# Performance work log

Measured on AMD Instinct MI355X. Metric: run time of the kernel, lower is better.

## Reference

```python
import jax, jax.numpy as jnp
import numpy as np

B, L, DM, DI, N = 8, 2048, 512, 768, 8  # batch, seq, d_model, d_inner=int(1.5*512), d_state


def setup_inputs() -> dict:
    key = jax.random.key(0)
    ks = jax.random.split(key, 8)
    g = lambda k, shape, sc=1.0: (jax.random.normal(k, shape, jnp.float32) * sc)
    return {
        "x": g(ks[0], (B, L, DM)),
        "W_in": g(ks[1], (DM, 2 * DI), 0.02),    # in_proj weight (stored in->out)
        "A_log": g(ks[2], (DI, N)),               # nn.Parameter(randn)
        "D_param": g(ks[3], (DI,)),               # skip-connection D
        "W_x": g(ks[4], (DI, N), 0.02),           # x_proj weight
        "W_dt": g(ks[5], (N, DI), 0.02),          # dt_proj weight
        "b_dt": jnp.zeros((DI,), jnp.float32),    # dt_proj bias
        "W_out": g(ks[6], (DI, DM), 0.02),        # out_proj weight
    }


def reference(x, W_in, A_log, D_param, W_x, W_dt, b_dt, W_out):
    xz = x @ W_in                                  # (B,L,2*DI)
    d_inner = W_in.shape[1] // 2
    x_ssm, z = xz[..., :d_inner], xz[..., d_inner:]
    x_ssm = jax.nn.silu(x_ssm)                     # (B,L,DI)
    A = -jnp.exp(A_log.astype(jnp.float32))        # (DI,N)
    delta = jax.nn.softplus((x_ssm @ W_x) @ W_dt + b_dt)  # (B,L,DI)

    n_state = A.shape[-1]

    def step(h, inp):
        xt, dt = inp                               # each (B,DI)
        dA = jnp.exp(dt[..., None] * A)            # (B,DI,N)
        h = dA * h + dt[..., None] * xt[..., None]
        y = jnp.sum(h, axis=-1) + D_param * xt     # (B,DI)
        return h, y

    h0 = jnp.zeros((x.shape[0], d_inner, n_state), x_ssm.dtype)
    xs = (jnp.swapaxes(x_ssm, 0, 1), jnp.swapaxes(delta, 0, 1))  # (L,B,DI)
    _, ys = jax.lax.scan(step, h0, xs)             # ys: (L,B,DI)
    y = jnp.swapaxes(ys, 0, 1)                     # (B,L,DI)
    y = y * jax.nn.silu(z)
    return y @ W_out                               # (B,L,DM)
```

## Files before the change

### kernel.cpp

```cpp
#include <hip/hip_runtime.h>

typedef unsigned short bfu;
typedef __attribute__((ext_vector_type(8))) short short8;
typedef __attribute__((ext_vector_type(4))) float f32x4;

__device__ __forceinline__ float bf2f(bfu u){
  union { unsigned int i; float f; } v; v.i = ((unsigned int)u) << 16; return v.f;
}
__device__ __forceinline__ bfu f2bf(float f){
  union { float f; unsigned int i; } v; v.f = f;
  unsigned int r = (v.i + 0x7FFFu + ((v.i >> 16) & 1u)) >> 16;
  return (bfu)r;
}
__device__ __forceinline__ float fexp2(float x){ return __builtin_amdgcn_exp2f(x); }
__device__ __forceinline__ float flog2(float x){ return __builtin_amdgcn_logf(x); }
__device__ __forceinline__ float softplusf(float x){
  float t = fexp2(-fabsf(x) * 1.44269504088896f);
  return fmaxf(x, 0.f) + 0.69314718055995f * flog2(1.f + t);
}
__device__ __forceinline__ void gload16(const bfu* g, bfu* l){
  __builtin_amdgcn_global_load_lds((const __attribute__((address_space(1))) unsigned int*)g,
                                   (__attribute__((address_space(3))) unsigned int*)l, 16, 0, 0);
}

__global__ __launch_bounds__(256) void cvt_all_kernel(const float* __restrict__ x, bfu* __restrict__ x_bf,
                                                      const float* __restrict__ W_in, const float* __restrict__ W_out,
                                                      const float* __restrict__ W_x,
                                                      bfu* __restrict__ WinT, bfu* __restrict__ WoutT,
                                                      float* __restrict__ WxT){
  int g = blockIdx.x * 256 + threadIdx.x;
  if (g < 2097152){
    float4 v = ((const float4*)x)[g];
    ushort4 o;
    o.x = f2bf(v.x); o.y = f2bf(v.y); o.z = f2bf(v.z); o.w = f2bf(v.w);
    ((ushort4*)x_bf)[g] = o;
    return;
  }
  int h = g - 2097152;
  if (h < 786432){
    int r = h % 512, c = h / 512;
    WinT[h] = f2bf(W_in[(size_t)r * 1536 + c]);
  } else if (h < 786432 + 393216){
    int h2 = h - 786432;
    int r = h2 % 768, c = h2 / 768;
    WoutT[h2] = f2bf(W_out[(size_t)r * 512 + c]);
  } else if (h < 786432 + 393216 + 6144){
    int h2 = h - (786432 + 393216);
    int n = h2 / 768, k = h2 % 768;
    WxT[h2] = W_x[(size_t)k * 8 + n];
  }
}

template<int EPI, int BM, int KK>
__global__ __launch_bounds__(BM * 2)
void gemm_sb(const bfu* __restrict__ Amat, const bfu* __restrict__ Bt,
             void* __restrict__ out0, void* __restrict__ out1,
             int NBN, int N)
{
  constexpr int BN = 128;
  constexpr int THREADS = BM * 2;
  constexpr int RPI = THREADS / 8;
  __shared__ bfu As[BM * 64];
  __shared__ bfu Bs[BN * 64];
  const int tid  = threadIdx.x;
  const int lane = tid & 63;
  const int w    = tid >> 6;
  const int wr   = w >> 1, wc = w & 1;

  const int cpx = gridDim.x >> 3;
  const int id  = blockIdx.x;
  const int nid = (id & 7) * cpx + (id >> 3);
  const int bn  = nid % NBN;
  const int bm  = nid / NBN;

  const int srow = tid >> 3;
  const int scol = ((tid & 7) ^ (srow & 7)) * 8;
  const bfu* gA = Amat + ((size_t)(bm * BM + srow)) * KK + scol;
  const bfu* gB = Bt   + ((size_t)(bn * BN + srow)) * KK + scol;
  bfu* lA = As + srow * 64 + (tid & 7) * 8;
  bfu* lB = Bs + srow * 64 + (tid & 7) * 8;

  f32x4 acc[4][4];
  #pragma unroll
  for (int i = 0; i < 4; i++)
    #pragma unroll
    for (int j = 0; j < 4; j++)
      #pragma unroll
      for (int r = 0; r < 4; r++) acc[i][j][r] = 0.f;

  for (int k0 = 0; k0 < KK; k0 += 64){
    #pragma unroll
    for (int i = 0; i < BM / RPI; i++)
      gload16(gA + (size_t)(i * RPI) * KK + k0, lA + i * RPI * 64);
    #pragma unroll
    for (int j = 0; j < BN / RPI; j++)
      gload16(gB + (size_t)(j * RPI) * KK + k0, lB + j * RPI * 64);
    __syncthreads();

    #pragma unroll
    for (int kk = 0; kk < 2; kk++){
      short8 a[4], b[4];
      const int sA = ((kk * 4 + (lane >> 4)) ^ (lane & 7)) * 8;
      #pragma unroll
      for (int m = 0; m < 4; m++){
        int r = wr * 64 + m * 16 + (lane & 15);
        a[m] = *(const short8*)&As[r * 64 + sA];
      }
      #pragma unroll
      for (int n = 0; n < 4; n++){
        int r = wc * 64 + n * 16 + (lane & 15);
        b[n] = *(const short8*)&Bs[r * 64 + sA];
      }
      #pragma unroll
      for (int m = 0; m < 4; m++)
        #pragma unroll
        for (int n = 0; n < 4; n++)
          acc[m][n] = __builtin_amdgcn_mfma_f32_16x16x32_bf16(a[m], b[n], acc[m][n], 0, 0, 0);
    }
    __syncthreads();
  }

  #pragma unroll
  for (int m = 0; m < 4; m++){
    #pragma unroll
    for (int n = 0; n < 4; n++){
      const int row0 = bm * BM + wr * 64 + m * 16 + (lane >> 4) * 4;
      const int col  = bn * BN + wc * 64 + n * 16 + (lane & 15);
      #pragma unroll
      for (int r = 0; r < 4; r++){
        float v = acc[m][n][r];
        int row = row0 + r;
        if (EPI == 0){
          float s = v / (1.f + __expf(-v));
          if (col < 768) ((bfu*)out0)[(size_t)row * 768 + col]         = f2bf(s);
          else           ((bfu*)out1)[(size_t)row * 768 + (col - 768)] = f2bf(s);
        } else {
          ((float*)out0)[(size_t)row * N + col] = v;
        }
      }
    }
  }
}

__global__ __launch_bounds__(256) void u_kernel(const bfu* __restrict__ xssm, const float* __restrict__ WxT,
                                                float* __restrict__ u){
  int wid = threadIdx.x >> 6, lane = threadIdx.x & 63;
  int row = blockIdx.x * 4 + wid;
  const bfu* xr = xssm + (size_t)row * 768;
  float acc[8];
  #pragma unroll
  for (int n = 0; n < 8; n++) acc[n] = 0.f;
  #pragma unroll
  for (int i = 0; i < 3; i++){
    int kb = i * 256 + lane * 4;
    ushort4 xq = *(const ushort4*)(xr + kb);
    float x0 = bf2f(xq.x), x1 = bf2f(xq.y), x2 = bf2f(xq.z), x3 = bf2f(xq.w);
    #pragma unroll
    for (int n = 0; n < 8; n++){
      float4 wv = *(const float4*)(WxT + (size_t)n * 768 + kb);
      acc[n] += x0 * wv.x + x1 * wv.y + x2 * wv.z + x3 * wv.w;
    }
  }
  #pragma unroll
  for (int n = 0; n < 8; n++){
    #pragma unroll
    for (int off = 32; off >= 1; off >>= 1) acc[n] += __shfl_xor(acc[n], off, 64);
  }
  if (lane == 0){
    float4 o0 = { acc[0], acc[1], acc[2], acc[3] };
    float4 o1 = { acc[4], acc[5], acc[6], acc[7] };
    *(float4*)(u + (size_t)row * 8)     = o0;
    *(float4*)(u + (size_t)row * 8 + 4) = o1;
  }
}

__global__ __launch_bounds__(128) void scan_phase1(const bfu* __restrict__ xssm, const float* __restrict__ u,
    const float* __restrict__ Wdt, const float* __restrict__ bdt, const float* __restrict__ A_log,
    float* __restrict__ Pws, float* __restrict__ Hws){
  int tid = threadIdx.x;
  int bid = blockIdx.x;
  int b = bid / 192; int rem = bid % 192;
  int c = rem / 3;   int dblk = rem % 3;
  int d0 = dblk * 256 + tid * 2;
  float Al2[2][8], H[2][8], Wr[2][8], bd[2], S[2];
  #pragma unroll
  for (int j = 0; j < 2; j++){
    bd[j] = bdt[d0 + j];
    S[j] = 0.f;
    #pragma unroll
    for (int n = 0; n < 8; n++){
      Al2[j][n] = -__expf(A_log[(size_t)(d0 + j) * 8 + n]) * 1.4426950408889634f;
      Wr[j][n]  = Wdt[(size_t)n * 768 + d0 + j];
      H[j][n] = 0.f;
    }
  }
  int r0 = b * 2048 + c * 32;
  size_t base = (size_t)r0 * 768 + d0;
  #pragma unroll 8
  for (int i = 0; i < 32; i++){
    float4 u0 = *(const float4*)(u + (size_t)(r0 + i) * 8);
    float4 u1 = *(const float4*)(u + (size_t)(r0 + i) * 8 + 4);
    ushort2 xq = *(const ushort2*)(xssm + base + (size_t)i * 768);
    #pragma unroll
    for (int j = 0; j < 2; j++){
      float xt = bf2f(j == 0 ? xq.x : xq.y);
      float dv = bd[j] + u0.x * Wr[j][0] + u0.y * Wr[j][1] + u0.z * Wr[j][2] + u0.w * Wr[j][3]
                       + u1.x * Wr[j][4] + u1.y * Wr[j][5] + u1.z * Wr[j][6] + u1.w * Wr[j][7];
      float dt = softplusf(dv);
      float dx = dt * xt;
      S[j] += dt;
      #pragma unroll
      for (int n = 0; n < 8; n++){
        float e = fexp2(dt * Al2[j][n]);
        H[j][n] = e * H[j][n] + dx;
      }
    }
  }
  size_t o = (((size_t)b * 64 + c) * 768 + d0) * 8;
  #pragma unroll
  for (int j = 0; j < 2; j++){
    float4 p0, p1;
    p0.x = fexp2(S[j] * Al2[j][0]); p0.y = fexp2(S[j] * Al2[j][1]);
    p0.z = fexp2(S[j] * Al2[j][2]); p0.w = fexp2(S[j] * Al2[j][3]);
    p1.x = fexp2(S[j] * Al2[j][4]); p1.y = fexp2(S[j] * Al2[j][5]);
    p1.z = fexp2(S[j] * Al2[j][6]); p1.w = fexp2(S[j] * Al2[j][7]);
    float4 h0 = { H[j][0], H[j][1], H[j][2], H[j][3] };
    float4 h1 = { H[j][4], H[j][5], H[j][6], H[j][7] };
    *(float4*)(Pws + o + j * 8)     = p0;
    *(float4*)(Pws + o + j * 8 + 4) = p1;
    *(float4*)(Hws + o + j * 8)     = h0;
    *(float4*)(Hws + o + j * 8 + 4) = h1;
  }
}

__global__ __launch_bounds__(256) void scan_phase2(float* __restrict__ Pws, const float* __restrict__ Hws){
  int g = blockIdx.x * 256 + threadIdx.x;
  int within = g % 6144;
  int b = g / 6144;
  size_t base = (size_t)b * 64 * 6144 + within;
  float hin = 0.f;
  #pragma unroll 8
  for (int c = 0; c < 64; c++){
    size_t idx = base + (size_t)c * 6144;
    float p = Pws[idx], hh = Hws[idx];
    Pws[idx] = hin;
    hin = p * hin + hh;
  }
}

__global__ __launch_bounds__(128) void scan_phase3(const bfu* __restrict__ xssm, const float* __restrict__ u,
    const float* __restrict__ Wdt, const float* __restrict__ bdt, const float* __restrict__ A_log,
    const float* __restrict__ Dp, const bfu* __restrict__ siluz, const float* __restrict__ Hin,
    bfu* __restrict__ yz){
  int tid = threadIdx.x;
  int bid = blockIdx.x;
  int b = bid / 192; int rem = bid % 192;
  int c = rem / 3;   int dblk = rem % 3;
  int d0 = dblk * 256 + tid * 2;
  float Al2[2][8], H[2][8], Wr[2][8], bd[2], Dd[2];
  size_t o = (((size_t)b * 64 + c) * 768 + d0) * 8;
  #pragma unroll
  for (int j = 0; j < 2; j++){
    bd[j] = bdt[d0 + j];
    Dd[j] = Dp[d0 + j];
    float4 h0 = *(const float4*)(Hin + o + j * 8);
    float4 h1 = *(const float4*)(Hin + o + j * 8 + 4);
    H[j][0] = h0.x; H[j][1] = h0.y; H[j][2] = h0.z; H[j][3] = h0.w;
    H[j][4] = h1.x; H[j][5] = h1.y; H[j][6] = h1.z; H[j][7] = h1.w;
    #pragma unroll
    for (int n = 0; n < 8; n++){
      Al2[j][n] = -__expf(A_log[(size_t)(d0 + j) * 8 + n]) * 1.4426950408889634f;
      Wr[j][n]  = Wdt[(size_t)n * 768 + d0 + j];
    }
  }
  int r0 = b * 2048 + c * 32;
  size_t base = (size_t)r0 * 768 + d0;
  #pragma unroll 8
  for (int i = 0; i < 32; i++){
    float4 u0 = *(const float4*)(u + (size_t)(r0 + i) * 8);
    float4 u1 = *(const float4*)(u + (size_t)(r0 + i) * 8 + 4);
    ushort2 xq = *(const ushort2*)(xssm + base + (size_t)i * 768);
    ushort2 zq = *(const ushort2*)(siluz + base + (size_t)i * 768);
    ushort2 oq;
    #pragma unroll
    for (int j = 0; j < 2; j++){
      float xt = bf2f(j == 0 ? xq.x : xq.y);
      float dv = bd[j] + u0.x * Wr[j][0] + u0.y * Wr[j][1] + u0.z * Wr[j][2] + u0.w * Wr[j][3]
                       + u1.x * Wr[j][4] + u1.y * Wr[j][5] + u1.z * Wr[j][6] + u1.w * Wr[j][7];
      float dt = softplusf(dv);
      float dx = dt * xt;
      float y = Dd[j] * xt;
      #pragma unroll
      for (int n = 0; n < 8; n++){
        float e = fexp2(dt * Al2[j][n]);
        H[j][n] = e * H[j][n] + dx;
        y += H[j][n];
      }
      float sz = bf2f(j == 0 ? zq.x : zq.y);
      bfu r = f2bf(y * sz);
      if (j == 0) oq.x = r; else oq.y = r;
    }
    *(ushort2*)(yz + base + (size_t)i * 768) = oq;
  }
}

extern "C" void kernel_launch(void* const* d_in, const int* in_sizes, int n_in,
                              void* d_out, int out_size, void* d_ws, size_t ws_size,
                              hipStream_t stream){
  const float* x     = (const float*)d_in[0];
  const float* W_in  = (const float*)d_in[1];
  const float* A_log = (const float*)d_in[2];
  const float* D_par = (const float*)d_in[3];
  const float* W_x   = (const float*)d_in[4];
  const float* W_dt  = (const float*)d_in[5];
  const float* b_dt  = (const float*)d_in[6];
  const float* W_out = (const float*)d_in[7];
  float* out = (float*)d_out;
  (void)in_sizes; (void)n_in; (void)out_size; (void)ws_size;

  char* base = (char*)d_ws;
  size_t off = 0;
  auto alloc = [&](size_t bytes)->char*{
    char* p = base + off; off += (bytes + 255) & ~(size_t)255; return p;
  };
  bfu*   x_bf  = (bfu*)  alloc((size_t)16384 * 512 * 2);
  bfu*   WinT  = (bfu*)  alloc((size_t)1536 * 512 * 2);
  bfu*   WoutT = (bfu*)  alloc((size_t)512 * 768 * 2);
  float* WxT   = (float*)alloc((size_t)8 * 768 * 4);
  bfu*   xssm  = (bfu*)  alloc((size_t)16384 * 768 * 2);
  bfu*   siluz = (bfu*)  alloc((size_t)16384 * 768 * 2);
  float* u     = (float*)alloc((size_t)16384 * 8 * 4);
  float* Pws   = (float*)alloc((size_t)8 * 64 * 768 * 8 * 4);
  float* Hws   = (float*)alloc((size_t)8 * 64 * 768 * 8 * 4);
  bfu*   yz    = (bfu*)  alloc((size_t)16384 * 768 * 2);

  cvt_all_kernel<<<12824, 256, 0, stream>>>(x, x_bf, W_in, W_out, W_x, WinT, WoutT, WxT);
  gemm_sb<0, 256, 512><<<768, 512, 0, stream>>>(x_bf, WinT, xssm, siluz, 12, 1536);
  u_kernel<<<4096, 256, 0, stream>>>(xssm, WxT, u);
  scan_phase1<<<1536, 128, 0, stream>>>(xssm, u, W_dt, b_dt, A_log, Pws, Hws);
  scan_phase2<<<192, 256, 0, stream>>>(Pws, Hws);
  scan_phase3<<<1536, 128, 0, stream>>>(xssm, u, W_dt, b_dt, A_log, D_par, siluz, Pws, yz);
  gemm_sb<1, 128, 768><<<512, 256, 0, stream>>>(yz, WoutT, out, nullptr, 4, 512);
}
```

Baseline: 163.2 us.

## Use 4-wave 256x128 GEMM tile for in_proj and batch scan phase2 loads

Adds a new in_proj GEMM kernel in which each of 4 waves computes a 128x64 output tile (8x4 MFMA fragments), instead of 8 waves over the same 256x128 block. This raises per-wave register reuse of the A and B fragments loaded from LDS, and the block is launched with 256 threads. Separately, scan_phase2 now loads 16 chunk values at a time before running the serial recurrence, so the global loads are issued together rather than chained. Risks: higher VGPR pressure from 128 accumulators per lane, which lowers occupancy, and the single-buffered k-loop has no overlap between loads and compute.

New measurement: 201.1 us. 23.2% more time.

```diff
diff --git a/kernel.cpp b/kernel.cpp
--- a/kernel.cpp
+++ b/kernel.cpp
@@ -48,6 +48,94 @@
     int h2 = h - (786432 + 393216);
     int n = h2 / 768, k = h2 % 768;
     WxT[h2] = W_x[(size_t)k * 8 + n];
+  }
+}
+
+template<int EPI, int KK>
+__global__ __launch_bounds__(256)
+void gemm_w4(const bfu* __restrict__ Amat, const bfu* __restrict__ Bt,
+             void* __restrict__ out0, void* __restrict__ out1,
+             int NBN, int N)
+{
+  __shared__ bfu As[256 * 64];
+  __shared__ bfu Bs[128 * 64];
+  const int tid  = threadIdx.x;
+  const int lane = tid & 63;
+  const int w    = tid >> 6;
+  const int wr   = w >> 1, wc = w & 1;
+
+  const int cpx = gridDim.x >> 3;
+  const int id  = blockIdx.x;
+  const int nid = (id & 7) * cpx + (id >> 3);
+  const int bn  = nid % NBN;
+  const int bm  = nid / NBN;
+
+  const int srow = tid >> 3;
+  const int scol = ((tid & 7) ^ (srow & 7)) * 8;
+  const bfu* gA = Amat + ((size_t)(bm * 256 + srow)) * KK + scol;
+  const bfu* gB = Bt   + ((size_t)(bn * 128 + srow)) * KK + scol;
+  bfu* lA = As + srow * 64 + (tid & 7) * 8;
+  bfu* lB = Bs + srow * 64 + (tid & 7) * 8;
+
+  f32x4 acc[8][4];
+  #pragma unroll
+  for (int i = 0; i < 8; i++)
+    #pragma unroll
+    for (int j = 0; j < 4; j++)
+      #pragma unroll
+      for (int r = 0; r < 4; r++) acc[i][j][r] = 0.f;
+
+  for (int k0 = 0; k0 < KK; k0 += 64){
+    #pragma unroll
+    for (int i = 0; i < 8; i++)
+      gload16(gA + (size_t)(i * 32) * KK + k0, lA + i * 32 * 64);
+    #pragma unroll
+    for (int j = 0; j < 4; j++)
+      gload16(gB + (size_t)(j * 32) * KK + k0, lB + j * 32 * 64);
+    __syncthreads();
+
+    #pragma unroll
+    for (int kk = 0; kk < 2; kk++){
+      short8 a[8], b[4];
+      const int sA = ((kk * 4 + (lane >> 4)) ^ (lane & 7)) * 8;
+      #pragma unroll
+      for (int m = 0; m < 8; m++){
+        int r = wr * 128 + m * 16 + (lane & 15);
+        a[m] = *(const short8*)&As[r * 64 + sA];
+      }
+      #pragma unroll
+      for (int n = 0; n < 4; n++){
+        int r = wc * 64 + n * 16 + (lane & 15);
+        b[n] = *(const short8*)&Bs[r * 64 + sA];
+      }
+      #pragma unroll
+      for (int m = 0; m < 8; m++)
+        #pragma unroll
+        for (int n = 0; n < 4; n++)
+          acc[m][n] = __builtin_amdgcn_mfma_f32_16x16x32_bf16(a[m], b[n], acc[m][n], 0, 0, 0);
+    }
+    __syncthreads();
+  }
+
+  #pragma unroll
+  for (int m = 0; m < 8; m++){
+    #pragma unroll
+    for (int n = 0; n < 4; n++){
+      const int row0 = bm * 256 + wr * 128 + m * 16 + (lane >> 4) * 4;
+      const int col  = bn * 128 + wc * 64 + n * 16 + (lane & 15);
+      #pragma unroll
+      for (int r = 0; r < 4; r++){
+        float v = acc[m][n][r];
+        int row = row0 + r;
+        if (EPI == 0){
+          float s = v / (1.f + __expf(-v));
+          if (col < 768) ((bfu*)out0)[(size_t)row * 768 + col]         = f2bf(s);
+          else           ((bfu*)out1)[(size_t)row * 768 + (col - 768)] = f2bf(s);
+        } else {
+          ((float*)out0)[(size_t)row * N + col] = v;
+        }
+      }
+    }
   }
 }
 
@@ -239,12 +327,21 @@
   int b = g / 6144;
   size_t base = (size_t)b * 64 * 6144 + within;
   float hin = 0.f;
-  #pragma unroll 8
-  for (int c = 0; c < 64; c++){
-    size_t idx = base + (size_t)c * 6144;
-    float p = Pws[idx], hh = Hws[idx];
-    Pws[idx] = hin;
-    hin = p * hin + hh;
+  float pv[16], hv[16];
+  #pragma unroll
+  for (int B = 0; B < 4; B++){
+    #pragma unroll
+    for (int i = 0; i < 16; i++){
+      size_t idx = base + (size_t)(B * 16 + i) * 6144;
+      pv[i] = Pws[idx];
+      hv[i] = Hws[idx];
+    }
+    #pragma unroll
+    for (int i = 0; i < 16; i++){
+      size_t idx = base + (size_t)(B * 16 + i) * 6144;
+      Pws[idx] = hin;
+      hin = pv[i] * hin + hv[i];
+    }
   }
 }
 
@@ -335,7 +432,7 @@
   bfu*   yz    = (bfu*)  alloc((size_t)16384 * 768 * 2);
 
   cvt_all_kernel<<<12824, 256, 0, stream>>>(x, x_bf, W_in, W_out, W_x, WinT, WoutT, WxT);
-  gemm_sb<0, 256, 512><<<768, 512, 0, stream>>>(x_bf, WinT, xssm, siluz, 12, 1536);
+  gemm_w4<0, 512><<<768, 256, 0, stream>>>(x_bf, WinT, xssm, siluz, 12, 1536);
   u_kernel<<<4096, 256, 0, stream>>>(xssm, WxT, u);
   scan_phase1<<<1536, 128, 0, stream>>>(xssm, u, W_dt, b_dt, A_log, Pws, Hws);
   scan_phase2<<<192, 256, 0, stream>>>(Pws, Hws);
```
